# Kernel tuning notes

Measured on AMD Instinct MI355X. Metric: run time of the kernel, lower is better.

Reference implementation:

```python
import jax, jax.numpy as jnp
import numpy as np

_LUM = jnp.array([0.299, 0.587, 0.114], dtype=jnp.float32)


def setup_inputs() -> dict:
    key = jax.random.key(0)
    k1, k2 = jax.random.split(key)
    B, H, W = 4, 1024, 1024
    grid = jax.random.normal(k1, (B, 12, 16, 16, 8), dtype=jnp.float32)
    image = jax.random.uniform(k2, (B, 3, H, W), dtype=jnp.float32)
    return {"grid": grid, "image": image}


def _trilinear_sample(G, x, y, z):
    """Faithful port of F.grid_sample (5D, bilinear, border, align_corners=True).

    G: (B, C, D, Hg, Wg). Coords in [-1,1]: x -> Wg axis, y -> Hg axis, z -> D axis.
    x, y, z: (B, H, W). Returns (B, H, W, C).
    """
    B, C, D, Hg, Wg = G.shape

    def unnorm(c, size):
        u = (c + 1.0) * 0.5 * (size - 1)  # align_corners=True
        return jnp.clip(u, 0.0, size - 1)  # border padding

    ux, uy, uz = unnorm(x, Wg), unnorm(y, Hg), unnorm(z, D)
    x0 = jnp.floor(ux).astype(jnp.int32)
    y0 = jnp.floor(uy).astype(jnp.int32)
    z0 = jnp.floor(uz).astype(jnp.int32)
    x1 = jnp.minimum(x0 + 1, Wg - 1)
    y1 = jnp.minimum(y0 + 1, Hg - 1)
    z1 = jnp.minimum(z0 + 1, D - 1)
    wx = (ux - x0)[..., None]
    wy = (uy - y0)[..., None]
    wz = (uz - z0)[..., None]

    Gt = jnp.transpose(G, (0, 2, 3, 4, 1))  # (B, D, Hg, Wg, C)
    bb = jnp.arange(B)[:, None, None]

    def g(zi, yi, xi):
        return Gt[bb, zi, yi, xi]  # (B, H, W, C)

    c00 = g(z0, y0, x0) * (1 - wx) + g(z0, y0, x1) * wx
    c01 = g(z0, y1, x0) * (1 - wx) + g(z0, y1, x1) * wx
    c10 = g(z1, y0, x0) * (1 - wx) + g(z1, y0, x1) * wx
    c11 = g(z1, y1, x0) * (1 - wx) + g(z1, y1, x1) * wx
    c0 = c00 * (1 - wy) + c01 * wy
    c1 = c10 * (1 - wy) + c11 * wy
    return c0 * (1 - wz) + c1 * wz


def reference(grid, image):
    B, C, H, W = image.shape
    out_ch, in_ch = 3, 3
    n_mat = out_ch * in_ch

    guide = jnp.einsum('bchw,c->bhw', image, _LUM)  # luminance guide
    gx = jnp.linspace(0.0, 1.0, W) * 2.0 - 1.0  # image x -> grid_sample x (last axis)
    gy = jnp.linspace(0.0, 1.0, H) * 2.0 - 1.0  # image y -> grid_sample y
    xb = jnp.broadcast_to(gx[None, None, :], (B, H, W))
    yb = jnp.broadcast_to(gy[None, :, None], (B, H, W))
    zb = guide * 2.0 - 1.0  # guide -> grid_sample z (depth axis)

    coeffs = _trilinear_sample(grid, xb, yb, zb)  # (B, H, W, 12)
    A = coeffs[..., :n_mat].reshape(B, H, W, out_ch, in_ch)
    bias = coeffs[..., n_mat:]  # (B, H, W, out_ch)

    img_hwc = jnp.transpose(image, (0, 2, 3, 1))  # (B, H, W, in_ch)
    out = jnp.einsum('bhwoi,bhwi->bhwo', A, img_hwc) + bias
    out = jnp.clip(out, 0.0, 1.0)
    return jnp.transpose(out, (0, 3, 1, 2))  # (B, out_ch, H, W)
```

## Files before the change

### kernel.cpp

```cpp
#include <hip/hip_runtime.h>

#define BB 4
#define HH 1024
#define WW 1024
#define NC 12
#define GD 16
#define GH 16
#define GW 8

#define ZS 52
#define XS (GD * ZS)
#define FSZ (GW * XS)

__global__ __launch_bounds__(256) void bgrid_row(const float* __restrict__ img,
                                                 const float* __restrict__ grid,
                                                 float* __restrict__ out)
{
    const int y = blockIdx.x;
    const int b = blockIdx.y;
    const int tid = threadIdx.x;

    __shared__ __align__(16) float F[FSZ];

    float uy = fminf(fmaxf(y * (15.0f / 1023.0f), 0.0f), 15.0f);
    int y0 = (int)uy;
    int y1 = min(y0 + 1, GH - 1);
    float wy = uy - (float)y0;

    const float* gb = grid + (size_t)b * (NC * GD * GH * GW);
#pragma unroll
    for (int j = 0; j < 6; j++) {
        int t = tid + 256 * j;
        int x = t & 7;
        int z = (t >> 3) & 15;
        int c = t >> 7;
        int gi = (c * GD + z) * (GH * GW) + x;
        float g0 = gb[gi + y0 * GW];
        float g1 = gb[gi + y1 * GW];
        F[x * XS + z * ZS + c] = g0 + wy * (g1 - g0);
    }
    __syncthreads();

    const size_t plane = (size_t)HH * WW;
    const size_t rowoff = (size_t)b * 3 * plane + (size_t)y * WW;
    const float4 r4 = *(const float4*)(img + rowoff + 4 * tid);
    const float4 g4 = *(const float4*)(img + rowoff + plane + 4 * tid);
    const float4 b4 = *(const float4*)(img + rowoff + 2 * plane + 4 * tid);

    float4 o0, o1, o2;
    float* o0p = (float*)&o0; float* o1p = (float*)&o1; float* o2p = (float*)&o2;
    const float* rp = (const float*)&r4;
    const float* gp = (const float*)&g4;
    const float* bp = (const float*)&b4;

#pragma unroll
    for (int p = 0; p < 4; p++) {
        const int px = 4 * tid + p;
        const float r = rp[p], g = gp[p], bl = bp[p];

        float ux = fminf(fmaxf(px * (7.0f / 1023.0f), 0.0f), 7.0f);
        int x0 = (int)ux;
        int x1 = min(x0 + 1, GW - 1);
        float wx = ux - (float)x0;

        float lum = 0.299f * r + 0.587f * g + 0.114f * bl;
        float uz = fminf(fmaxf(lum * 15.0f, 0.0f), 15.0f);
        int z0 = (int)uz;
        int z1 = min(z0 + 1, GD - 1);
        float wz = uz - (float)z0;

        const float* f00 = &F[x0 * XS + z0 * ZS];
        const float* f10 = &F[x1 * XS + z0 * ZS];
        const float* f01 = &F[x0 * XS + z1 * ZS];
        const float* f11 = &F[x1 * XS + z1 * ZS];

        float cf[12];
#pragma unroll
        for (int q = 0; q < 3; q++) {
            const float4 a = *(const float4*)(f00 + 4 * q);
            const float4 bq = *(const float4*)(f10 + 4 * q);
            const float4 c = *(const float4*)(f01 + 4 * q);
            const float4 d = *(const float4*)(f11 + 4 * q);
            float m0x = a.x + wx * (bq.x - a.x), m1x = c.x + wx * (d.x - c.x);
            float m0y = a.y + wx * (bq.y - a.y), m1y = c.y + wx * (d.y - c.y);
            float m0z = a.z + wx * (bq.z - a.z), m1z = c.z + wx * (d.z - c.z);
            float m0w = a.w + wx * (bq.w - a.w), m1w = c.w + wx * (d.w - c.w);
            cf[4 * q + 0] = m0x + wz * (m1x - m0x);
            cf[4 * q + 1] = m0y + wz * (m1y - m0y);
            cf[4 * q + 2] = m0z + wz * (m1z - m0z);
            cf[4 * q + 3] = m0w + wz * (m1w - m0w);
        }

        float v0 = cf[0] * r + cf[1] * g + cf[2] * bl + cf[9];
        float v1 = cf[3] * r + cf[4] * g + cf[5] * bl + cf[10];
        float v2 = cf[6] * r + cf[7] * g + cf[8] * bl + cf[11];
        o0p[p] = fminf(fmaxf(v0, 0.0f), 1.0f);
        o1p[p] = fminf(fmaxf(v1, 0.0f), 1.0f);
        o2p[p] = fminf(fmaxf(v2, 0.0f), 1.0f);
    }

    *(float4*)(out + rowoff + 4 * tid) = o0;
    *(float4*)(out + rowoff + plane + 4 * tid) = o1;
    *(float4*)(out + rowoff + 2 * plane + 4 * tid) = o2;
}

extern "C" void kernel_launch(void* const* d_in, const int* in_sizes, int n_in,
                              void* d_out, int out_size, void* d_ws, size_t ws_size,
                              hipStream_t stream) {
    const float* grid  = (const float*)d_in[0];
    const float* image = (const float*)d_in[1];
    float* out = (float*)d_out;

    dim3 blk(256);
    dim3 grd(HH, BB);
    bgrid_row<<<grd, blk, 0, stream>>>(image, grid, out);
}
```

Before: 24.23 us.

## Pack z-neighbour grid pairs as fp16 in LDS to halve shared-memory reads

Shared memory now stores each grid cell as a half2 pair holding the y-interpolated values at z and z+1. Each pixel therefore needs two 48-byte LDS reads (x0 and x1) instead of four. The z-lerp runs in fp16 and the result is widened to float before the x-lerp. This reduces LDS bandwidth and instruction count per pixel, at the cost of fp16 precision error in the coefficients, which could exceed tolerance. Two redundant lower clamps are also removed.

```diff
diff --git a/kernel.cpp b/kernel.cpp
--- a/kernel.cpp
+++ b/kernel.cpp
@@ -8,9 +8,19 @@
 #define GH 16
 #define GW 8
 
-#define ZS 52
-#define XS (GD * ZS)
-#define FSZ (GW * XS)
+#define ZSD 12
+#define XSD 196
+#define HSZ (GW * XSD)
+
+typedef _Float16 half2v __attribute__((ext_vector_type(2)));
+
+__device__ __forceinline__ float zlerp(uint u, _Float16 wzh) {
+    union { uint v; half2v h; } c;
+    c.v = u;
+    _Float16 lo = c.h.x, hi = c.h.y;
+    _Float16 r = lo + wzh * (hi - lo);
+    return (float)r;
+}
 
 __global__ __launch_bounds__(256) void bgrid_row(const float* __restrict__ img,
                                                  const float* __restrict__ grid,
@@ -20,9 +30,9 @@
     const int b = blockIdx.y;
     const int tid = threadIdx.x;
 
-    __shared__ __align__(16) float F[FSZ];
+    __shared__ __align__(16) uint H[HSZ];
 
-    float uy = fminf(fmaxf(y * (15.0f / 1023.0f), 0.0f), 15.0f);
+    float uy = fminf(y * (15.0f / 1023.0f), 15.0f);
     int y0 = (int)uy;
     int y1 = min(y0 + 1, GH - 1);
     float wy = uy - (float)y0;
@@ -34,10 +44,17 @@
         int x = t & 7;
         int z = (t >> 3) & 15;
         int c = t >> 7;
-        int gi = (c * GD + z) * (GH * GW) + x;
-        float g0 = gb[gi + y0 * GW];
-        float g1 = gb[gi + y1 * GW];
-        F[x * XS + z * ZS + c] = g0 + wy * (g1 - g0);
+        int zp = min(z + 1, GD - 1);
+        const float* bc = gb + (size_t)c * (GD * GH * GW) + x;
+        float a0 = bc[z  * (GH * GW) + y0 * GW];
+        float a1 = bc[z  * (GH * GW) + y1 * GW];
+        float c0 = bc[zp * (GH * GW) + y0 * GW];
+        float c1 = bc[zp * (GH * GW) + y1 * GW];
+        float f0 = fmaf(wy, a1 - a0, a0);
+        float f1 = fmaf(wy, c1 - c0, c0);
+        union { half2v h; uint u; } pk;
+        pk.h = half2v{(_Float16)f0, (_Float16)f1};
+        H[x * XSD + z * ZSD + c] = pk.u;
     }
     __syncthreads();
 
@@ -58,7 +75,7 @@
         const int px = 4 * tid + p;
         const float r = rp[p], g = gp[p], bl = bp[p];
 
-        float ux = fminf(fmaxf(px * (7.0f / 1023.0f), 0.0f), 7.0f);
+        float ux = fminf(px * (7.0f / 1023.0f), 7.0f);
         int x0 = (int)ux;
         int x1 = min(x0 + 1, GW - 1);
         float wx = ux - (float)x0;
@@ -66,29 +83,27 @@
         float lum = 0.299f * r + 0.587f * g + 0.114f * bl;
         float uz = fminf(fmaxf(lum * 15.0f, 0.0f), 15.0f);
         int z0 = (int)uz;
-        int z1 = min(z0 + 1, GD - 1);
         float wz = uz - (float)z0;
+        _Float16 wzh = (_Float16)wz;
 
-        const float* f00 = &F[x0 * XS + z0 * ZS];
-        const float* f10 = &F[x1 * XS + z0 * ZS];
-        const float* f01 = &F[x0 * XS + z1 * ZS];
-        const float* f11 = &F[x1 * XS + z1 * ZS];
+        const int bx0 = x0 * XSD + z0 * ZSD;
+        const int bx1 = x1 * XSD + z0 * ZSD;
+        const uint4* qa = (const uint4*)&H[bx0];
+        const uint4* qb = (const uint4*)&H[bx1];
+        uint va[12], vb[12];
+        *(uint4*)(va + 0) = qa[0];
+        *(uint4*)(va + 4) = qa[1];
+        *(uint4*)(va + 8) = qa[2];
+        *(uint4*)(vb + 0) = qb[0];
+        *(uint4*)(vb + 4) = qb[1];
+        *(uint4*)(vb + 8) = qb[2];
 
         float cf[12];
 #pragma unroll
-        for (int q = 0; q < 3; q++) {
-            const float4 a = *(const float4*)(f00 + 4 * q);
-            const float4 bq = *(const float4*)(f10 + 4 * q);
-            const float4 c = *(const float4*)(f01 + 4 * q);
-            const float4 d = *(const float4*)(f11 + 4 * q);
-            float m0x = a.x + wx * (bq.x - a.x), m1x = c.x + wx * (d.x - c.x);
-            float m0y = a.y + wx * (bq.y - a.y), m1y = c.y + wx * (d.y - c.y);
-            float m0z = a.z + wx * (bq.z - a.z), m1z = c.z + wx * (d.z - c.z);
-            float m0w = a.w + wx * (bq.w - a.w), m1w = c.w + wx * (d.w - c.w);
-            cf[4 * q + 0] = m0x + wz * (m1x - m0x);
-            cf[4 * q + 1] = m0y + wz * (m1y - m0y);
-            cf[4 * q + 2] = m0z + wz * (m1z - m0z);
-            cf[4 * q + 3] = m0w + wz * (m1w - m0w);
+        for (int c = 0; c < 12; c++) {
+            float v0 = zlerp(va[c], wzh);
+            float v1 = zlerp(vb[c], wzh);
+            cf[c] = fmaf(wx, v1 - v0, v0);
         }
 
         float v0 = cf[0] * r + cf[1] * g + cf[2] * bl + cf[9];
```

Measured after the change: 28.83 us. 19.0% more time.
